# Optimization experiments

Measured on AMD Instinct MI355X. Metric: run time of the kernel, lower is better.

The kernel has to match this reference:

```python
import jax, jax.numpy as jnp
import numpy as np

DIM = 1024
DIM_HEAD = 64
HEADS = DIM // DIM_HEAD
WINDOW = 32
EPS = 1e-5


def setup_inputs() -> dict:
    key = jax.random.key(0)
    k0, k1, k2 = jax.random.split(key, 3)
    B, T = 2, 2048
    x = jax.random.normal(k0, (B, T, DIM), dtype=jnp.float32)
    ln_w = jnp.ones((DIM,), dtype=jnp.float32)
    ln_b = jnp.zeros((DIM,), dtype=jnp.float32)
    # torch nn.Linear weight layout: [out_features, in_features]
    w_qkv = jax.random.normal(k1, (3 * DIM, DIM), dtype=jnp.float32) * (1.0 / np.sqrt(DIM))
    w_out = jax.random.normal(k2, (DIM, DIM), dtype=jnp.float32) * (1.0 / np.sqrt(DIM))
    return {"x": x, "ln_w": ln_w, "ln_b": ln_b, "w_qkv": w_qkv, "w_out": w_out}


def _rotate_half(x):
    # reshape(..., 2, d/2) -> (-x2, x1), i.e. GPT-NeoX half rotation
    x1, x2 = jnp.split(x, 2, axis=-1)
    return jnp.concatenate((-x2, x1), axis=-1)


def reference(x, ln_w, ln_b, w_qkv, w_out):
    B, T, C = x.shape
    residual = x

    # LayerNorm (biased variance, eps=1e-5)
    mu = jnp.mean(x, axis=-1, keepdims=True)
    var = jnp.mean(jnp.square(x - mu), axis=-1, keepdims=True)
    xn = (x - mu) * jax.lax.rsqrt(var + EPS) * ln_w + ln_b

    qkv = xn @ w_qkv.T  # [B,T,3C]
    q, k, v = jnp.split(qkv, 3, axis=-1)
    def to_heads(t):
        return t.reshape(B, T, HEADS, DIM_HEAD).transpose(0, 2, 1, 3)  # [B,H,T,Dh]
    q, k, v = to_heads(q), to_heads(k), to_heads(v)

    # Sinusoidal RoPE freqs: [T, Dh] (freqs duplicated across halves)
    inv_freq = 1.0 / (10000.0 ** (jnp.arange(0, DIM_HEAD, 2, dtype=jnp.float32) / DIM_HEAD))
    t_pos = jnp.arange(T, dtype=jnp.float32)
    freqs = t_pos[:, None] * inv_freq[None, :]
    freqs = jnp.concatenate((freqs, freqs), axis=-1)  # [T, Dh]
    cos, sin = jnp.cos(freqs), jnp.sin(freqs)
    q = q * cos + _rotate_half(q) * sin
    k = k * cos + _rotate_half(k) * sin

    # Sliding-window causal mask: i >= j and i - j < WINDOW
    pos = jnp.arange(T)
    mask = (pos[:, None] >= pos[None, :]) & ((pos[:, None] - pos[None, :]) < WINDOW)

    scale = 1.0 / np.sqrt(DIM_HEAD)
    scores = jnp.einsum("bhqd,bhkd->bhqk", q, k) * scale
    scores = jnp.where(mask, scores, jnp.float32(-1e30))
    attn = jax.nn.softmax(scores, axis=-1)
    out = jnp.einsum("bhqk,bhkd->bhqd", attn, v)  # [B,H,T,Dh]

    out = out.transpose(0, 2, 1, 3).reshape(B, T, C) @ w_out.T
    return out + residual
```

## Files before the change

### kernel.cpp

```cpp
#include <hip/hip_runtime.h>
#include <hip/hip_bf16.h>
#include <math.h>

#define DIM 1024
#define HEADS 16
#define DH 64
#define WINDOW 32
#define TSEQ 2048
#define BB 2
#define ROWS (BB * TSEQ)
#define NQKV (3 * DIM)

typedef __bf16 bf16x8 __attribute__((ext_vector_type(8)));
typedef unsigned short u16x8 __attribute__((ext_vector_type(8)));
typedef float f32x4 __attribute__((ext_vector_type(4)));

__device__ __forceinline__ unsigned short f2bf(float f) {
  unsigned int u = __float_as_uint(f);
  u += 0x7fffu + ((u >> 16) & 1u);
  return (unsigned short)(u >> 16);
}

__device__ __forceinline__ void glds16(const void* g, void* l) {
  __builtin_amdgcn_global_load_lds((const __attribute__((address_space(1))) void*)g,
                                   (__attribute__((address_space(3))) void*)l,
                                   16, 0, 0);
}

__global__ void cvt_bf16(const float* __restrict__ in, unsigned short* __restrict__ out, int n4) {
  int i = blockIdx.x * blockDim.x + threadIdx.x;
  if (i < n4) {
    float4 v = *(const float4*)&in[(size_t)i * 4];
    ushort4 o = make_ushort4(f2bf(v.x), f2bf(v.y), f2bf(v.z), f2bf(v.w));
    *(ushort4*)&out[(size_t)i * 4] = o;
  }
}

__global__ void rope_tab(float* __restrict__ ctab, float* __restrict__ stab) {
  int idx = blockIdx.x * blockDim.x + threadIdx.x;
  int t = idx >> 5, i = idx & 31;
  float inv = powf(10000.0f, -(float)i / 32.0f);
  float f = (float)t * inv;
  float sv, cv;
  sincosf(f, &sv, &cv);
  ctab[idx] = cv;
  stab[idx] = sv;
}

__global__ __launch_bounds__(256) void ln_kernel(
    const float* __restrict__ x, const float* __restrict__ lw,
    const float* __restrict__ lb, unsigned short* __restrict__ xn) {
  const int row = blockIdx.x;
  const int c = threadIdx.x * 4;
  const float4 v = *(const float4*)&x[(size_t)row * DIM + c];
  float s = v.x + v.y + v.z + v.w;
  float s2 = v.x * v.x + v.y * v.y + v.z * v.z + v.w * v.w;
#pragma unroll
  for (int m = 32; m; m >>= 1) {
    s += __shfl_xor(s, m);
    s2 += __shfl_xor(s2, m);
  }
  __shared__ float ps[4], ps2[4];
  if ((threadIdx.x & 63) == 0) {
    ps[threadIdx.x >> 6] = s;
    ps2[threadIdx.x >> 6] = s2;
  }
  __syncthreads();
  s = ps[0] + ps[1] + ps[2] + ps[3];
  s2 = ps2[0] + ps2[1] + ps2[2] + ps2[3];
  const float mu = s * (1.0f / DIM);
  const float rs = rsqrtf(s2 * (1.0f / DIM) - mu * mu + 1e-5f);
  const float4 wv = *(const float4*)&lw[c];
  const float4 bv = *(const float4*)&lb[c];
  ushort4 o = make_ushort4(f2bf((v.x - mu) * rs * wv.x + bv.x),
                           f2bf((v.y - mu) * rs * wv.y + bv.y),
                           f2bf((v.z - mu) * rs * wv.z + bv.z),
                           f2bf((v.w - mu) * rs * wv.w + bv.w));
  *(ushort4*)&xn[(size_t)row * DIM + c] = o;
}

template<int MODE>
__global__ __launch_bounds__(256) void gemm_bt(
    const unsigned short* __restrict__ A, const unsigned short* __restrict__ B,
    float* __restrict__ Cf, unsigned short* __restrict__ Cb,
    const float* __restrict__ resid,
    const float* __restrict__ ctab, const float* __restrict__ stab,
    int M, int N, int K) {
  __shared__ unsigned short Al[128 * 32];
  __shared__ unsigned short Bl[128 * 32];
  const int t = threadIdx.x;
  const int lane = t & 63;
  const int wave = t >> 6;
  const int wm = wave >> 1;
  const int wn = wave & 1;
  const int bm = blockIdx.y * 128;
  const int bn = blockIdx.x * 128;

  f32x4 acc[4][4] = {};

  const int srow = t >> 2;
  const int scol = (t & 3) * 8;
  const unsigned short* ga = A + (size_t)(bm + srow) * K + scol;
  const unsigned short* gb = B + (size_t)(bn + srow) * K + scol;
  unsigned short* la = Al + (t & ~63) * 8;
  unsigned short* lb = Bl + (t & ~63) * 8;

  const int fr = lane & 15;
  const int fko = (lane >> 4) * 8;

  for (int k0 = 0; k0 < K; k0 += 32) {
    __syncthreads();
    glds16(ga + k0, la);
    glds16(ga + (size_t)64 * K + k0, la + 64 * 32);
    glds16(gb + k0, lb);
    glds16(gb + (size_t)64 * K + k0, lb + 64 * 32);
    __syncthreads();
    bf16x8 af[4], bfr[4];
#pragma unroll
    for (int i = 0; i < 4; ++i)
      af[i] = *(const bf16x8*)&Al[(wm * 64 + i * 16 + fr) * 32 + fko];
#pragma unroll
    for (int j = 0; j < 4; ++j)
      bfr[j] = *(const bf16x8*)&Bl[(wn * 64 + j * 16 + fr) * 32 + fko];
#pragma unroll
    for (int i = 0; i < 4; ++i)
#pragma unroll
      for (int j = 0; j < 4; ++j)
        acc[i][j] = __builtin_amdgcn_mfma_f32_16x16x32_bf16(af[i], bfr[j], acc[i][j], 0, 0, 0);
  }

  const int cr = (lane >> 4) * 4;
  const int cc = lane & 15;
  if (MODE == 0) {
#pragma unroll
    for (int i = 0; i < 4; ++i)
#pragma unroll
      for (int j = 0; j < 4; ++j)
#pragma unroll
        for (int r = 0; r < 4; ++r) {
          int row = bm + wm * 64 + i * 16 + cr + r;
          int col = bn + wn * 64 + j * 16 + cc;
          size_t idx = (size_t)row * N + col;
          Cf[idx] = acc[i][j][r] + resid[idx];
        }
  } else {
    const int ctype = bn >> 10;
#pragma unroll
    for (int i = 0; i < 4; ++i)
#pragma unroll
      for (int r = 0; r < 4; ++r) {
        const int row = bm + wm * 64 + i * 16 + cr + r;
        const int pos = row & (TSEQ - 1);
        if (ctype == 2) {
#pragma unroll
          for (int j = 0; j < 4; ++j) {
            int col = bn + wn * 64 + j * 16 + cc;
            Cb[(size_t)row * N + col] = f2bf(acc[i][j][r]);
          }
        } else {
#pragma unroll
          for (int j = 0; j < 2; ++j) {
            int col = bn + wn * 64 + j * 16 + cc;
            float cv = ctab[pos * 32 + j * 16 + cc];
            float sv = stab[pos * 32 + j * 16 + cc];
            float lo = acc[i][j][r], hi = acc[i][j + 2][r];
            float olo = lo * cv - hi * sv;
            float ohi = hi * cv + lo * sv;
            if (ctype == 0) { olo *= 0.125f; ohi *= 0.125f; }
            Cb[(size_t)row * N + col] = f2bf(olo);
            Cb[(size_t)row * N + col + 32] = f2bf(ohi);
          }
        }
      }
  }
}

#define KST 72
#define VST 104
#define PST 72
__global__ __launch_bounds__(256) void attn_kernel(const unsigned short* __restrict__ qkv,
                                                   unsigned short* __restrict__ out) {
  __shared__ unsigned short Kb[96 * KST];
  __shared__ unsigned short Vt[64 * VST];
  __shared__ unsigned short Pl[64 * PST];
  const int qtile = blockIdx.x;
  const int bh = blockIdx.y;
  const int b = bh >> 4, h = bh & 15;
  const int qs = qtile * 64;
  const int t = threadIdx.x;

  for (int e = t; e < 768; e += 256) {
    int r = e >> 3, seg = e & 7;
    int j = qs - 32 + r;
    u16x8 kv = {};
    if (j >= 0)
      kv = *(const u16x8*)&qkv[((size_t)(b * TSEQ + j)) * NQKV + DIM + h * 64 + seg * 8];
    *(u16x8*)&Kb[r * KST + seg * 8] = kv;
  }
  for (int e = t; e < 768; e += 256) {
    int r = e >> 3, seg = e & 7;
    int j = qs - 32 + r;
    u16x8 vv = {};
    if (j >= 0)
      vv = *(const u16x8*)&qkv[((size_t)(b * TSEQ + j)) * NQKV + 2 * DIM + h * 64 + seg * 8];
#pragma unroll
    for (int u = 0; u < 8; ++u) Vt[(seg * 8 + u) * VST + r] = vv[u];
  }
  for (int e = t; e < 64 * PST / 8; e += 256)
    *(u16x8*)&Pl[e * 8] = (u16x8){};
  __syncthreads();

  const int wave = t >> 6;
  const int lane = t & 63;
  const int fr = lane & 15;
  const int fko = (lane >> 4) * 8;
  const int g = lane >> 4;
  const int cc = lane & 15;
  const int kmin = 32 - qs - wave * 16;

  const unsigned short* qrow = qkv + ((size_t)(b * TSEQ + qs + wave * 16 + fr)) * NQKV + h * 64;
  bf16x8 qf0 = *(const bf16x8*)&qrow[fko];
  bf16x8 qf1 = *(const bf16x8*)&qrow[32 + fko];

  f32x4 sc[3] = {};
#pragma unroll
  for (int kt = 0; kt < 3; ++kt) {
    const unsigned short* kb = &Kb[(wave * 16 + kt * 16 + fr) * KST];
    bf16x8 kf0 = *(const bf16x8*)&kb[fko];
    bf16x8 kf1 = *(const bf16x8*)&kb[32 + fko];
    sc[kt] = __builtin_amdgcn_mfma_f32_16x16x32_bf16(qf0, kf0, sc[kt], 0, 0, 0);
    sc[kt] = __builtin_amdgcn_mfma_f32_16x16x32_bf16(qf1, kf1, sc[kt], 0, 0, 0);
  }

#pragma unroll
  for (int reg = 0; reg < 4; ++reg) {
    const int r = g * 4 + reg;
    float sv[3];
    bool va[3];
    float mx = -1e30f;
#pragma unroll
    for (int kt = 0; kt < 3; ++kt) {
      int kk = kt * 16 + cc;
      bool valid = (kk >= r + 1) && (kk <= r + 32) && (kk >= kmin);
      va[kt] = valid;
      sv[kt] = valid ? sc[kt][reg] : -1e30f;
      mx = fmaxf(mx, sv[kt]);
    }
#pragma unroll
    for (int mm = 8; mm; mm >>= 1) mx = fmaxf(mx, __shfl_xor(mx, mm));
    float pe[3], sum = 0.f;
#pragma unroll
    for (int kt = 0; kt < 3; ++kt) {
      pe[kt] = va[kt] ? __expf(sv[kt] - mx) : 0.f;
      sum += pe[kt];
    }
#pragma unroll
    for (int mm = 8; mm; mm >>= 1) sum += __shfl_xor(sum, mm);
    float rinv = 1.0f / sum;
#pragma unroll
    for (int kt = 0; kt < 3; ++kt)
      Pl[(wave * 16 + r) * PST + kt * 16 + cc] = f2bf(pe[kt] * rinv);
  }

  const unsigned short* prow = &Pl[(wave * 16 + fr) * PST];
  bf16x8 pf0 = *(const bf16x8*)&prow[fko];
  bf16x8 pf1 = *(const bf16x8*)&prow[32 + fko];
  f32x4 o[4] = {};
#pragma unroll
  for (int nt = 0; nt < 4; ++nt) {
    const unsigned short* vrow = &Vt[(nt * 16 + fr) * VST + wave * 16];
    bf16x8 vf0 = *(const bf16x8*)&vrow[fko];
    bf16x8 vf1 = *(const bf16x8*)&vrow[32 + fko];
    o[nt] = __builtin_amdgcn_mfma_f32_16x16x32_bf16(pf0, vf0, o[nt], 0, 0, 0);
    o[nt] = __builtin_amdgcn_mfma_f32_16x16x32_bf16(pf1, vf1, o[nt], 0, 0, 0);
  }

#pragma unroll
  for (int nt = 0; nt < 4; ++nt)
#pragma unroll
    for (int reg = 0; reg < 4; ++reg) {
      int qg = qs + wave * 16 + g * 4 + reg;
      out[((size_t)(b * TSEQ + qg)) * DIM + h * 64 + nt * 16 + cc] = f2bf(o[nt][reg]);
    }
}

extern "C" void kernel_launch(void* const* d_in, const int* in_sizes, int n_in,
                              void* d_out, int out_size, void* d_ws, size_t ws_size,
                              hipStream_t stream) {
  const float* x    = (const float*)d_in[0];
  const float* lw   = (const float*)d_in[1];
  const float* lbp  = (const float*)d_in[2];
  const float* wqkv = (const float*)d_in[3];
  const float* wout = (const float*)d_in[4];
  float* out = (float*)d_out;

  char* w = (char*)d_ws;
  unsigned short* xn   = (unsigned short*)(w);
  unsigned short* wqb  = (unsigned short*)(w + 8388608);
  unsigned short* wob  = (unsigned short*)(w + 14680064);
  unsigned short* atb  = (unsigned short*)(w + 16777216);
  float* ctab = (float*)(w + 25165824);
  float* stab = (float*)(w + 25427968);
  unsigned short* qkvb = (unsigned short*)(w + 25690112);

  cvt_bf16<<<3072, 256, 0, stream>>>(wqkv, wqb, 786432);
  cvt_bf16<<<1024, 256, 0, stream>>>(wout, wob, 262144);
  rope_tab<<<256, 256, 0, stream>>>(ctab, stab);
  ln_kernel<<<ROWS, 256, 0, stream>>>(x, lw, lbp, xn);
  gemm_bt<1><<<dim3(24, 32), 256, 0, stream>>>(xn, wqb, nullptr, qkvb, nullptr,
                                               ctab, stab, ROWS, NQKV, DIM);
  attn_kernel<<<dim3(32, 32), 256, 0, stream>>>(qkvb, atb);
  gemm_bt<0><<<dim3(8, 32), 256, 0, stream>>>(atb, wob, out, nullptr, x,
                                              nullptr, nullptr, ROWS, DIM, DIM);
}
```

Before: 101.0 us.

## Replace QKV GEMM with 256x256 double-buffered 8-wave pipelined kernel and merge prep launches

```diff
diff --git a/kernel.cpp b/kernel.cpp
--- a/kernel.cpp
+++ b/kernel.cpp
@@ -27,24 +27,28 @@
                                    16, 0, 0);
 }
 
-__global__ void cvt_bf16(const float* __restrict__ in, unsigned short* __restrict__ out, int n4) {
-  int i = blockIdx.x * blockDim.x + threadIdx.x;
-  if (i < n4) {
+__global__ __launch_bounds__(256) void prep_kernel(
+    const float* __restrict__ wqkv, const float* __restrict__ wout,
+    unsigned short* __restrict__ wqb, unsigned short* __restrict__ wob,
+    float* __restrict__ ctab, float* __restrict__ stab) {
+  int bid = blockIdx.x;
+  if (bid < 4096) {
+    const float* in = (bid < 3072) ? wqkv : wout;
+    unsigned short* outp = (bid < 3072) ? wqb : wob;
+    int i = (bid < 3072 ? bid : bid - 3072) * 256 + threadIdx.x;
     float4 v = *(const float4*)&in[(size_t)i * 4];
     ushort4 o = make_ushort4(f2bf(v.x), f2bf(v.y), f2bf(v.z), f2bf(v.w));
-    *(ushort4*)&out[(size_t)i * 4] = o;
-  }
-}
-
-__global__ void rope_tab(float* __restrict__ ctab, float* __restrict__ stab) {
-  int idx = blockIdx.x * blockDim.x + threadIdx.x;
-  int t = idx >> 5, i = idx & 31;
-  float inv = powf(10000.0f, -(float)i / 32.0f);
-  float f = (float)t * inv;
-  float sv, cv;
-  sincosf(f, &sv, &cv);
-  ctab[idx] = cv;
-  stab[idx] = sv;
+    *(ushort4*)&outp[(size_t)i * 4] = o;
+  } else {
+    int idx = (bid - 4096) * 256 + threadIdx.x;
+    int t = idx >> 5, i = idx & 31;
+    float inv = powf(10000.0f, -(float)i / 32.0f);
+    float f = (float)t * inv;
+    float sv, cv;
+    sincosf(f, &sv, &cv);
+    ctab[idx] = cv;
+    stab[idx] = sv;
+  }
 }
 
 __global__ __launch_bounds__(256) void ln_kernel(
@@ -79,13 +83,140 @@
   *(ushort4*)&xn[(size_t)row * DIM + c] = o;
 }
 
-template<int MODE>
-__global__ __launch_bounds__(256) void gemm_bt(
+#define QKV_K 1024
+#define QKV_N 3072
+
+#define SA(NB, NT, Q) do { \
+    glds16(A + (size_t)(bm + 0 * 128 + (Q) * 64 + srow) * QKV_K + (NT) * 64 + scolw, \
+           &AQ[NB][Q][0 * 4096 + ldst]); \
+    glds16(A + (size_t)(bm + 1 * 128 + (Q) * 64 + srow) * QKV_K + (NT) * 64 + scolw, \
+           &AQ[NB][Q][1 * 4096 + ldst]); \
+  } while (0)
+#define SB(NB, NT, Q) do { \
+    glds16(B + (size_t)(bn + (0 * 2 + (t >> 8)) * 64 + (Q) * 32 + ((t >> 3) & 31)) * QKV_K + (NT) * 64 + scolw, \
+           &BQ[NB][Q][0 * 4096 + ldst]); \
+    glds16(B + (size_t)(bn + (1 * 2 + (t >> 8)) * 64 + (Q) * 32 + ((t >> 3) & 31)) * QKV_K + (NT) * 64 + scolw, \
+           &BQ[NB][Q][1 * 4096 + ldst]); \
+  } while (0)
+
+#define VM4 asm volatile("s_waitcnt vmcnt(4)" ::: "memory")
+#define VM0 asm volatile("s_waitcnt vmcnt(0)" ::: "memory")
+#define VMNONE do {} while (0)
+#define SNONE do {} while (0)
+
+#define PHASE(NB, QM, QN, STG, VMW) do { \
+    bf16x8 af[4][2], bq[2][2]; \
+    _Pragma("unroll") \
+    for (int mi = 0; mi < 4; ++mi) { \
+      const int ra = wm * 64 + mi * 16 + fr; \
+      const int cx = ((ra >> 2) & 1) << 4; \
+      af[mi][0] = *(const bf16x8*)&AQ[NB][QM][ra * 64 + (fko ^ cx)]; \
+      af[mi][1] = *(const bf16x8*)&AQ[NB][QM][ra * 64 + 32 + (fko ^ cx)]; \
+    } \
+    _Pragma("unroll") \
+    for (int nj = 0; nj < 2; ++nj) { \
+      const int rb = wn * 32 + nj * 16 + fr; \
+      const int cx = ((rb >> 2) & 1) << 4; \
+      bq[nj][0] = *(const bf16x8*)&BQ[NB][QN][rb * 64 + (fko ^ cx)]; \
+      bq[nj][1] = *(const bf16x8*)&BQ[NB][QN][rb * 64 + 32 + (fko ^ cx)]; \
+    } \
+    STG; \
+    __builtin_amdgcn_s_barrier(); \
+    asm volatile("s_waitcnt lgkmcnt(0)" ::: "memory"); \
+    __builtin_amdgcn_sched_barrier(0); \
+    __builtin_amdgcn_s_setprio(1); \
+    _Pragma("unroll") \
+    for (int ks = 0; ks < 2; ++ks) \
+      _Pragma("unroll") \
+      for (int mi = 0; mi < 4; ++mi) \
+        _Pragma("unroll") \
+        for (int nj = 0; nj < 2; ++nj) \
+          acc[(QM) * 4 + mi][(QN) * 2 + nj] = __builtin_amdgcn_mfma_f32_16x16x32_bf16( \
+              af[mi][ks], bq[nj][ks], acc[(QM) * 4 + mi][(QN) * 2 + nj], 0, 0, 0); \
+    __builtin_amdgcn_s_setprio(0); \
+    VMW; \
+    __builtin_amdgcn_s_barrier(); \
+  } while (0)
+
+#define TILE(NB, NBX, NT1) do { \
+    PHASE(NB, 0, 0, SA(NBX, NT1, 0), VM4); \
+    PHASE(NB, 0, 1, SB(NBX, NT1, 0), VM4); \
+    PHASE(NB, 1, 0, SB(NBX, NT1, 1), VMNONE); \
+    PHASE(NB, 1, 1, SA(NBX, NT1, 1), VM4); \
+  } while (0)
+
+__global__ __launch_bounds__(512, 2) void gemm_qkv8(
     const unsigned short* __restrict__ A, const unsigned short* __restrict__ B,
-    float* __restrict__ Cf, unsigned short* __restrict__ Cb,
-    const float* __restrict__ resid,
-    const float* __restrict__ ctab, const float* __restrict__ stab,
-    int M, int N, int K) {
+    unsigned short* __restrict__ Cb,
+    const float* __restrict__ ctab, const float* __restrict__ stab) {
+  __shared__ unsigned short AQ[2][2][8192];
+  __shared__ unsigned short BQ[2][2][8192];
+  const int t = threadIdx.x;
+  const int lane = t & 63;
+  const int wave = t >> 6;
+  const int wm = wave >> 2;
+  const int wn = wave & 3;
+  const int bm = blockIdx.y * 256;
+  const int bn = blockIdx.x * 256;
+  const int fr = lane & 15;
+  const int fko = (lane >> 4) * 8;
+
+  f32x4 acc[8][4] = {};
+
+  const int srow = t >> 3;
+  const int scolw = ((t & 7) * 8) ^ (((t >> 5) & 1) << 4);
+  const int ldst = (t & ~63) * 8;
+
+  SA(0, 0, 0); SB(0, 0, 0); SB(0, 0, 1); SA(0, 0, 1);
+  VM4;
+  __builtin_amdgcn_s_barrier();
+
+  for (int tt = 0; tt < 14; tt += 2) {
+    TILE(0, 1, tt + 1);
+    TILE(1, 0, tt + 2);
+  }
+  TILE(0, 1, 15);
+  PHASE(1, 0, 0, SNONE, VM0);
+  PHASE(1, 0, 1, SNONE, VMNONE);
+  PHASE(1, 1, 0, SNONE, VMNONE);
+  PHASE(1, 1, 1, SNONE, VMNONE);
+
+  const int cr = (lane >> 4) * 4;
+  const int cc = lane & 15;
+  const int ctype = bn >> 10;
+#pragma unroll
+  for (int m = 0; m < 8; ++m) {
+#pragma unroll
+    for (int rr = 0; rr < 4; ++rr) {
+      const int row = bm + wm * 128 + m * 16 + cr + rr;
+      const int pos = row & (TSEQ - 1);
+      if (ctype == 2) {
+#pragma unroll
+        for (int n = 0; n < 4; ++n) {
+          const int col = bn + wn * 64 + n * 16 + cc;
+          Cb[(size_t)row * QKV_N + col] = f2bf(acc[m][n][rr]);
+        }
+      } else {
+#pragma unroll
+        for (int n = 0; n < 2; ++n) {
+          const int col = bn + wn * 64 + n * 16 + cc;
+          const float cv = ctab[pos * 32 + n * 16 + cc];
+          const float sv = stab[pos * 32 + n * 16 + cc];
+          float lo = acc[m][n][rr], hi = acc[m][n + 2][rr];
+          float olo = lo * cv - hi * sv;
+          float ohi = hi * cv + lo * sv;
+          if (ctype == 0) { olo *= 0.125f; ohi *= 0.125f; }
+          Cb[(size_t)row * QKV_N + col] = f2bf(olo);
+          Cb[(size_t)row * QKV_N + col + 32] = f2bf(ohi);
+        }
+      }
+    }
+  }
+}
+
+__global__ __launch_bounds__(256) void gemm_proj(
+    const unsigned short* __restrict__ A, const unsigned short* __restrict__ B,
+    float* __restrict__ Cf, const float* __restrict__ resid, int M, int N, int K) {
   __shared__ unsigned short Al[128 * 32];
   __shared__ unsigned short Bl[128 * 32];
   const int t = threadIdx.x;
@@ -131,48 +262,17 @@
 
   const int cr = (lane >> 4) * 4;
   const int cc = lane & 15;
-  if (MODE == 0) {
-#pragma unroll
-    for (int i = 0; i < 4; ++i)
-#pragma unroll
-      for (int j = 0; j < 4; ++j)
-#pragma unroll
-        for (int r = 0; r < 4; ++r) {
-          int row = bm + wm * 64 + i * 16 + cr + r;
-          int col = bn + wn * 64 + j * 16 + cc;
-          size_t idx = (size_t)row * N + col;
-          Cf[idx] = acc[i][j][r] + resid[idx];
-        }
-  } else {
-    const int ctype = bn >> 10;
-#pragma unroll
-    for (int i = 0; i < 4; ++i)
+#pragma unroll
+  for (int i = 0; i < 4; ++i)
+#pragma unroll
+    for (int j = 0; j < 4; ++j)
 #pragma unroll
       for (int r = 0; r < 4; ++r) {
-        const int row = bm + wm * 64 + i * 16 + cr + r;
-        const int pos = row & (TSEQ - 1);
-        if (ctype == 2) {
-#pragma unroll
-          for (int j = 0; j < 4; ++j) {
-            int col = bn + wn * 64 + j * 16 + cc;
-            Cb[(size_t)row * N + col] = f2bf(acc[i][j][r]);
-          }
-        } else {
-#pragma unroll
-          for (int j = 0; j < 2; ++j) {
-            int col = bn + wn * 64 + j * 16 + cc;
-            float cv = ctab[pos * 32 + j * 16 + cc];
-            float sv = stab[pos * 32 + j * 16 + cc];
-            float lo = acc[i][j][r], hi = acc[i][j + 2][r];
-            float olo = lo * cv - hi * sv;
-            float ohi = hi * cv + lo * sv;
-            if (ctype == 0) { olo *= 0.125f; ohi *= 0.125f; }
-            Cb[(size_t)row * N + col] = f2bf(olo);
-            Cb[(size_t)row * N + col + 32] = f2bf(ohi);
-          }
-        }
+        int row = bm + wm * 64 + i * 16 + cr + r;
+        int col = bn + wn * 64 + j * 16 + cc;
+        size_t idx = (size_t)row * N + col;
+        Cf[idx] = acc[i][j][r] + resid[idx];
       }
-  }
 }
 
 #define KST 72
@@ -303,13 +403,9 @@
   float* stab = (float*)(w + 25427968);
   unsigned short* qkvb = (unsigned short*)(w + 25690112);
 
-  cvt_bf16<<<3072, 256, 0, stream>>>(wqkv, wqb, 786432);
-  cvt_bf16<<<1024, 256, 0, stream>>>(wout, wob, 262144);
-  rope_tab<<<256, 256, 0, stream>>>(ctab, stab);
+  prep_kernel<<<4352, 256, 0, stream>>>(wqkv, wout, wqb, wob, ctab, stab);
   ln_kernel<<<ROWS, 256, 0, stream>>>(x, lw, lbp, xn);
-  gemm_bt<1><<<dim3(24, 32), 256, 0, stream>>>(xn, wqb, nullptr, qkvb, nullptr,
-                                               ctab, stab, ROWS, NQKV, DIM);
+  gemm_qkv8<<<dim3(12, 16), 512, 0, stream>>>(xn, wqb, qkvb, ctab, stab);
   attn_kernel<<<dim3(32, 32), 256, 0, stream>>>(qkvb, atb);
-  gemm_bt<0><<<dim3(8, 32), 256, 0, stream>>>(atb, wob, out, nullptr, x,
-                                              nullptr, nullptr, ROWS, DIM, DIM);
-}
+  gemm_proj<<<dim3(8, 32), 256, 0, stream>>>(atb, wob, out, x, ROWS, DIM, DIM);
+}
```

New measurement: 111.7 us. +10.6%, slower.
